# Performance work log

Measured on AMD Instinct MI355X. Metric: run time of the kernel, lower is better.

## Reference

```python
import jax, jax.numpy as jnp
import numpy as np

N = 100000   # nodes
E = 800000   # directed edges
G = 1000     # graphs
D = 128      # latent_dim
F_IN = 64    # num_node_feats
K = 3        # max_k
BLOCKS = 3   # max_block
H = 5        # multi_h_emb_weight
EPS = 1e-5


def _bn(x, g, b):
    # BatchNorm1d in training mode: biased batch variance
    m = x.mean(axis=0)
    v = x.var(axis=0)
    return (x - m) * jax.lax.rsqrt(v + EPS) * g + b


def setup_inputs() -> dict:
    key = jax.random.key(0)
    ks = jax.random.split(key, 12)
    inp = {
        'node_feat': jax.random.normal(ks[0], (N, F_IN), dtype=jnp.float32),
        'src': jax.random.randint(ks[1], (E,), 0, N),
        'dst': jax.random.randint(ks[2], (E,), 0, N),
        'seg': jnp.sort(jax.random.randint(ks[3], (N,), 0, G)),
        'node_W': jax.random.normal(ks[4], (F_IN, D), dtype=jnp.float32) * 0.05,
        'node_b': jnp.zeros((D,), jnp.float32),
        'bn1_g': jnp.ones((D,), jnp.float32),
        'bn1_b': jnp.zeros((D,), jnp.float32),
        'conv_W': jax.random.normal(ks[5], (K, D, D), dtype=jnp.float32) * 0.05,
        'conv_b': jnp.zeros((K, D), jnp.float32),
        'bn2_g': jnp.ones((K, D), jnp.float32),
        'bn2_b': jnp.zeros((K, D), jnp.float32),
        'k_weight': jax.random.normal(ks[6], (K * D, D), dtype=jnp.float32) * 0.05,
        'bn3_g': jnp.ones((D,), jnp.float32),
        'bn3_b': jnp.zeros((D,), jnp.float32),
        'attn_W1': jax.random.normal(ks[7], (D, D), dtype=jnp.float32) * 0.05,
        'attn_b1': jnp.zeros((D,), jnp.float32),
        'bna_g': jnp.ones((D,), jnp.float32),
        'bna_b': jnp.zeros((D,), jnp.float32),
        'attn_W2': jax.random.normal(ks[8], (D, H), dtype=jnp.float32) * 0.05,
        'attn_b2': jnp.zeros((H,), jnp.float32),
        'bnb_g': jnp.ones((H,), jnp.float32),
        'bnb_b': jnp.zeros((H,), jnp.float32),
    }
    return inp


def reference(node_feat, src, dst, seg,
              node_W, node_b, bn1_g, bn1_b,
              conv_W, conv_b, bn2_g, bn2_b,
              k_weight, bn3_g, bn3_b,
              attn_W1, attn_b1, bna_g, bna_b,
              attn_W2, attn_b2, bnb_g, bnb_b):
    def spmm(x):
        # torch.spmm(A, x) with unweighted n2n adjacency: out[dst] += x[src]
        return jax.ops.segment_sum(x[src], dst, num_segments=N)

    # node embedding: Linear + BN + ReLU
    inp = jax.nn.relu(_bn(node_feat @ node_W + node_b, bn1_g, bn1_b))

    cur = inp
    for block in range(BLOCKS):
        block_input = cur if block == 0 else cur + inp
        # multi_hop: K chained spmm + Linear + BN, concatenated
        input_x = block_input
        outs = []
        for k in range(K):
            pooled = spmm(input_x) + block_input
            input_x = _bn(pooled @ conv_W[k] + conv_b[k], bn2_g[k], bn2_b[k])
            outs.append(input_x)
        result = jnp.concatenate(outs, axis=-1)          # [N, K*D]
        cur = jax.nn.relu(_bn(result @ k_weight, bn3_g, bn3_b))

    node_emb = cur                                       # [N, D]

    # APooling: per-node softmax over heads, segment-wise weighted sum
    a = jnp.tanh(node_emb @ attn_W1 + attn_b1)
    a = _bn(a, bna_g, bna_b)
    a = a @ attn_W2 + attn_b2
    a = _bn(a, bnb_g, bnb_b)                             # [N, H]
    alpha = jax.nn.softmax(a, axis=-1)                   # softmax over head dim (dim=-1)
    # graph_emb[g, h, d] = sum_{n in graph g} alpha[n, h] * node_emb[n, d]
    graph_emb = jax.ops.segment_sum(alpha[:, :, None] * node_emb[:, None, :],
                                    seg, num_segments=G)  # [G, H, D]
    h_out = jax.nn.relu(graph_emb.reshape(G, H * D))

    # L1 regularizer over params with dim > 1, divided by number of graphs
    reg = (jnp.abs(node_W).sum() + jnp.abs(conv_W).sum() + jnp.abs(k_weight).sum()
           + jnp.abs(attn_W1).sum() + jnp.abs(attn_W2).sum())
    return h_out, reg / G
```

## Files before the change

kernel.cpp:

```cpp
#include <hip/hip_runtime.h>
#include <hip/hip_bf16.h>

#define D128 128
#define EPS 1e-5f

typedef unsigned short bfl;
typedef __bf16 bf16x8 __attribute__((ext_vector_type(8)));
typedef float f32x4 __attribute__((ext_vector_type(4)));

__device__ inline float bf2f(unsigned short u) { return __uint_as_float(((unsigned int)u) << 16); }
__device__ inline unsigned short f2bf(float f) {
    unsigned int x = __float_as_uint(f);
    return (unsigned short)((x + 0x7fffu + ((x >> 16) & 1u)) >> 16);
}

__global__ void dag_count_rank(const int* __restrict__ dst, int E,
                               int* __restrict__ deg, int* __restrict__ rank) {
    int i = blockIdx.x * blockDim.x + threadIdx.x;
    int stride = gridDim.x * blockDim.x;
    for (; i < E; i += stride) {
        int r = atomicAdd(&deg[dst[i]], 1);
        rank[i] = r;
    }
}

__global__ void dag_scan1(const int* __restrict__ deg, int N, int* __restrict__ out, int* __restrict__ partials) {
    __shared__ int sdata[256];
    int t = threadIdx.x;
    int base = blockIdx.x * 1024 + t * 4;
    int v[4]; int s = 0;
#pragma unroll
    for (int j = 0; j < 4; j++) { int idx = base + j; v[j] = (idx < N) ? deg[idx] : 0; s += v[j]; }
    sdata[t] = s; __syncthreads();
    for (int off = 1; off < 256; off <<= 1) {
        int x = (t >= off) ? sdata[t - off] : 0;
        __syncthreads();
        sdata[t] += x;
        __syncthreads();
    }
    int run = (t == 0) ? 0 : sdata[t - 1];
#pragma unroll
    for (int j = 0; j < 4; j++) { int idx = base + j; if (idx < N) out[idx] = run; run += v[j]; }
    if (t == 255) partials[blockIdx.x] = sdata[255];
}

__global__ void dag_scan2(int* __restrict__ partials, int P) {
    __shared__ int sdata[256];
    int t = threadIdx.x;
    int v = (t < P) ? partials[t] : 0;
    sdata[t] = v; __syncthreads();
    for (int off = 1; off < 256; off <<= 1) {
        int x = (t >= off) ? sdata[t - off] : 0;
        __syncthreads();
        sdata[t] += x;
        __syncthreads();
    }
    if (t < P) partials[t] = sdata[t] - v;
}

__global__ void dag_scan3(int* __restrict__ rowptr, const int* __restrict__ partials, int N, int E) {
    int i = blockIdx.x * blockDim.x + threadIdx.x;
    int stride = gridDim.x * blockDim.x;
    for (; i < N; i += stride) rowptr[i] += partials[i >> 10];
    if (blockIdx.x == 0 && threadIdx.x == 0) rowptr[N] = E;
}

__global__ void dag_place(const int* __restrict__ src, const int* __restrict__ dst,
                          const int* __restrict__ rank, const int* __restrict__ rowptr,
                          int E, int* __restrict__ csr_src) {
    int i = blockIdx.x * blockDim.x + threadIdx.x;
    int stride = gridDim.x * blockDim.x;
    for (; i < E; i += stride) {
        csr_src[rowptr[dst[i]] + rank[i]] = src[i];
    }
}

__global__ void dag_wconv(const float* __restrict__ node_W, const float* __restrict__ conv_W,
                          const float* __restrict__ k_weight, const float* __restrict__ attn_W1,
                          bfl* __restrict__ wt) {
    int i = blockIdx.x * blockDim.x + threadIdx.x;
    if (i >= 122880) return;
    float v;
    if (i < 8192) {
        int n = i >> 6, k = i & 63;
        v = node_W[k * 128 + n];
    } else if (i < 8192 + 49152) {
        int j = i - 8192; int k = j >> 14; int r = j & 16383;
        int n = r >> 7, kk = r & 127;
        v = conv_W[k * 16384 + kk * 128 + n];
    } else if (i < 8192 + 98304) {
        int j = i - 8192 - 49152; int k = j >> 14; int r = j & 16383;
        int n = r >> 7, kk = r & 127;
        v = k_weight[(k * 128 + kk) * 128 + n];
    } else {
        int j = i - 8192 - 98304;
        int n = j >> 7, kk = j & 127;
        v = attn_W1[kk * 128 + n];
    }
    wt[i] = f2bf(v);
}

template<bool KWPREP>
__global__ void dag_finalize(float* __restrict__ part,
                             const float* __restrict__ g, const float* __restrict__ b,
                             float invN, float* __restrict__ slot,
                             const bfl* __restrict__ WtIn, bfl* __restrict__ Wt2,
                             float* __restrict__ bias2) {
    int t = threadIdx.x;
    float acc = 0.f;
#pragma unroll
    for (int i = 0; i < 8; i++) acc += part[i * 256 + t];
#pragma unroll
    for (int i = 0; i < 8; i++) part[i * 256 + t] = 0.f;
    __shared__ float sums[256];
    __shared__ float scs[128], shs[128];
    sums[t] = acc;
    __syncthreads();
    if (t < 128) {
        float m = sums[t] * invN;
        float var = sums[128 + t] * invN - m * m;
        float scale = g[t] * rsqrtf(var + EPS);
        float shift = b[t] - m * scale;
        scs[t] = scale; shs[t] = shift;
        slot[t] = scale; slot[128 + t] = shift;
    }
    if constexpr (KWPREP) {
        __syncthreads();
        int row = t >> 1, half = t & 1;
        const bfl* wr = WtIn + row * 128 + half * 64;
        bfl* w2 = Wt2 + row * 128 + half * 64;
        float a = 0.f;
        for (int k = 0; k < 64; k += 8) {
            bf16x8 v = *(const bf16x8*)(wr + k);
            bfl o[8];
#pragma unroll
            for (int j = 0; j < 8; j++) {
                float f = (float)v[j];
                int kk = half * 64 + k + j;
                a += shs[kk] * f;
                o[j] = f2bf(scs[kk] * f);
            }
            *(bf16x8*)(w2 + k) = *(bf16x8*)o;
        }
        a += __shfl_xor(a, 1);
        if (half == 0) bias2[row] = a;
    }
}

template<int KSTEPS, int XMODE, bool BIAS, bool TANH, bool ACC, bool STATS>
__global__ __launch_bounds__(256) void gemm_rw(
        const void* __restrict__ Xv, const bfl* __restrict__ Wt,
        const float* __restrict__ bias, bfl* __restrict__ Y,
        int Nrows, float* __restrict__ partOut) {
    const int Kdim = KSTEPS * 32;
    int t = threadIdx.x;
    int lane = t & 63;
    int wave = t >> 6;
    int cg = wave & 1, rg = wave >> 1;
    int l15 = lane & 15, lg = lane >> 4;

    bf16x8 af[4][KSTEPS];
#pragma unroll
    for (int nf = 0; nf < 4; nf++)
#pragma unroll
        for (int ks = 0; ks < KSTEPS; ks++)
            af[nf][ks] = *(const bf16x8*)(Wt + (size_t)(cg * 64 + nf * 16 + l15) * Kdim + ks * 32 + lg * 8);

    float bia[4][4];
    if (BIAS) {
#pragma unroll
        for (int nf = 0; nf < 4; nf++) {
            float4 bb = *(const float4*)(bias + cg * 64 + nf * 16 + lg * 4);
            bia[nf][0] = bb.x; bia[nf][1] = bb.y; bia[nf][2] = bb.z; bia[nf][3] = bb.w;
        }
    }

    float s_c[4][4], q_c[4][4];
    if constexpr (STATS) {
#pragma unroll
        for (int nf = 0; nf < 4; nf++)
#pragma unroll
            for (int j = 0; j < 4; j++) { s_c[nf][j] = 0.f; q_c[nf][j] = 0.f; }
    }

    const int RT = (Nrows + 15) >> 4;
    const int step = gridDim.x * 2;

    auto load_bf = [&](int rt, bf16x8* bfo) {
        int r = rt * 16 + l15;
        bool valid = (rt < RT) && (r < Nrows);
#pragma unroll
        for (int ks = 0; ks < KSTEPS; ks++) {
            if (valid) {
                if (XMODE == 0) {
                    bfo[ks] = *(const bf16x8*)((const bfl*)Xv + (size_t)r * Kdim + ks * 32 + lg * 8);
                } else {
                    const float* xp = (const float*)Xv + (size_t)r * Kdim + ks * 32 + lg * 8;
                    float4 a4 = *(const float4*)xp;
                    float4 b4 = *(const float4*)(xp + 4);
                    bf16x8 bb;
                    bb[0] = (__bf16)a4.x; bb[1] = (__bf16)a4.y; bb[2] = (__bf16)a4.z; bb[3] = (__bf16)a4.w;
                    bb[4] = (__bf16)b4.x; bb[5] = (__bf16)b4.y; bb[6] = (__bf16)b4.z; bb[7] = (__bf16)b4.w;
                    bfo[ks] = bb;
                }
            } else {
                bf16x8 bb;
#pragma unroll
                for (int j = 0; j < 8; j++) bb[j] = (__bf16)0.f;
                bfo[ks] = bb;
            }
        }
    };

    auto compute_store = [&](int rt, const bf16x8* bfc) {
        int r = rt * 16 + l15;
        bool valid = (rt < RT) && (r < Nrows);
        f32x4 acc[4];
#pragma unroll
        for (int nf = 0; nf < 4; nf++) acc[nf] = (f32x4)0.f;
#pragma unroll
        for (int ks = 0; ks < KSTEPS; ks++)
#pragma unroll
            for (int nf = 0; nf < 4; nf++)
                acc[nf] = __builtin_amdgcn_mfma_f32_16x16x32_bf16(af[nf][ks], bfc[ks], acc[nf], 0, 0, 0);
#pragma unroll
        for (int nf = 0; nf < 4; nf++) {
            int c0 = cg * 64 + nf * 16 + lg * 4;
            f32x4 v = acc[nf];
            if (BIAS) {
#pragma unroll
                for (int j = 0; j < 4; j++) v[j] += bia[nf][j];
            }
            if (TANH) {
#pragma unroll
                for (int j = 0; j < 4; j++) v[j] = tanhf(v[j]);
            }
            if (valid) {
                bfl* yp = Y + (size_t)r * D128 + c0;
                if (ACC) {
                    ushort4 old = *(const ushort4*)yp;
                    v[0] += bf2f(old.x); v[1] += bf2f(old.y); v[2] += bf2f(old.z); v[3] += bf2f(old.w);
                }
                ushort4 o;
                o.x = f2bf(v[0]); o.y = f2bf(v[1]); o.z = f2bf(v[2]); o.w = f2bf(v[3]);
                *(ushort4*)yp = o;
            }
            if constexpr (STATS) {
#pragma unroll
                for (int j = 0; j < 4; j++) {
                    float f = valid ? v[j] : 0.f;
                    s_c[nf][j] += f;
                    q_c[nf][j] += f * f;
                }
            }
        }
    };

    for (int rt = blockIdx.x * 2 + rg; rt < RT; rt += 2 * step) {
        bf16x8 bfA[KSTEPS], bfB[KSTEPS];
        load_bf(rt, bfA);
        load_bf(rt + step, bfB);
        compute_store(rt, bfA);
        compute_store(rt + step, bfB);
    }

    if constexpr (STATS) {
#pragma unroll
        for (int nf = 0; nf < 4; nf++)
#pragma unroll
            for (int j = 0; j < 4; j++) {
                float s = s_c[nf][j], q = q_c[nf][j];
                s += __shfl_xor(s, 1); s += __shfl_xor(s, 2); s += __shfl_xor(s, 4); s += __shfl_xor(s, 8);
                q += __shfl_xor(q, 1); q += __shfl_xor(q, 2); q += __shfl_xor(q, 4); q += __shfl_xor(q, 8);
                s_c[nf][j] = s; q_c[nf][j] = q;
            }
        __shared__ float red[2][2][64];
        ((float*)red)[t] = 0.f;
        __syncthreads();
        if (l15 == 0) {
#pragma unroll
            for (int nf = 0; nf < 4; nf++)
#pragma unroll
                for (int j = 0; j < 4; j++) {
                    int c = nf * 16 + lg * 4 + j;
                    atomicAdd(&red[cg][0][c], s_c[nf][j]);
                    atomicAdd(&red[cg][1][c], q_c[nf][j]);
                }
        }
        __syncthreads();
        int cgi = t >> 7, stat = (t >> 6) & 1, c = t & 63;
        atomicAdd(&partOut[(size_t)(blockIdx.x & 7) * 256 + stat * 128 + cgi * 64 + c],
                  red[cgi][stat][c]);
    }
}

__global__ __launch_bounds__(256) void dag_spmm(
        const bfl* __restrict__ x, const bfl* __restrict__ bi,
        const int* __restrict__ rowptr, const int* __restrict__ csr_src,
        bfl* __restrict__ out, int N, const float* __restrict__ scsh) {
    int t = threadIdx.x;
    int lane = t & 63;
    int wave = t >> 6;
    int l16 = lane & 15;
    int sub = lane >> 4;
    int c0 = l16 * 8;
    int n = blockIdx.x * 16 + wave * 4 + sub;
    bool valid = n < N;

    float sc[8], sh[8];
    if (scsh) {
        float4 a = *(const float4*)(scsh + c0);
        float4 b = *(const float4*)(scsh + c0 + 4);
        float4 p = *(const float4*)(scsh + 128 + c0);
        float4 q = *(const float4*)(scsh + 128 + c0 + 4);
        sc[0] = a.x; sc[1] = a.y; sc[2] = a.z; sc[3] = a.w;
        sc[4] = b.x; sc[5] = b.y; sc[6] = b.z; sc[7] = b.w;
        sh[0] = p.x; sh[1] = p.y; sh[2] = p.z; sh[3] = p.w;
        sh[4] = q.x; sh[5] = q.y; sh[6] = q.z; sh[7] = q.w;
    } else {
#pragma unroll
        for (int j = 0; j < 8; j++) { sc[j] = 1.f; sh[j] = 0.f; }
    }

    int p0 = valid ? rowptr[n] : 0;
    int p1 = valid ? rowptr[n + 1] : 0;
    int deg = p1 - p0;
    int md = deg;
    md = max(md, __shfl_xor(md, 16));
    md = max(md, __shfl_xor(md, 32));

    uint4 ub = make_uint4(0, 0, 0, 0);
    if (valid) ub = *(const uint4*)(bi + (size_t)n * D128 + c0);

    const bfl* xb = x + c0;
    float acc[8];
#pragma unroll
    for (int j = 0; j < 8; j++) acc[j] = 0.f;

    for (int j = 0; j < md; j += 4) {
        uint4 u[4];
#pragma unroll
        for (int r = 0; r < 4; r++) {
            u[r] = make_uint4(0, 0, 0, 0);
            if (j + r < deg) {
                int s = csr_src[p0 + j + r];
                u[r] = *(const uint4*)(xb + (size_t)s * D128);
            }
        }
#pragma unroll
        for (int r = 0; r < 4; r++) {
            acc[0] += __uint_as_float(u[r].x << 16);
            acc[1] += __uint_as_float(u[r].x & 0xffff0000u);
            acc[2] += __uint_as_float(u[r].y << 16);
            acc[3] += __uint_as_float(u[r].y & 0xffff0000u);
            acc[4] += __uint_as_float(u[r].z << 16);
            acc[5] += __uint_as_float(u[r].z & 0xffff0000u);
            acc[6] += __uint_as_float(u[r].w << 16);
            acc[7] += __uint_as_float(u[r].w & 0xffff0000u);
        }
    }

    if (valid) {
        float cnt = (float)deg;
        float bv[8];
        bv[0] = __uint_as_float(ub.x << 16); bv[1] = __uint_as_float(ub.x & 0xffff0000u);
        bv[2] = __uint_as_float(ub.y << 16); bv[3] = __uint_as_float(ub.y & 0xffff0000u);
        bv[4] = __uint_as_float(ub.z << 16); bv[5] = __uint_as_float(ub.z & 0xffff0000u);
        bv[6] = __uint_as_float(ub.w << 16); bv[7] = __uint_as_float(ub.w & 0xffff0000u);
        float v[8];
#pragma unroll
        for (int j = 0; j < 8; j++) v[j] = sc[j] * acc[j] + cnt * sh[j] + bv[j];
        uint4 o;
        o.x = (unsigned int)f2bf(v[0]) | ((unsigned int)f2bf(v[1]) << 16);
        o.y = (unsigned int)f2bf(v[2]) | ((unsigned int)f2bf(v[3]) << 16);
        o.z = (unsigned int)f2bf(v[4]) | ((unsigned int)f2bf(v[5]) << 16);
        o.w = (unsigned int)f2bf(v[6]) | ((unsigned int)f2bf(v[7]) << 16);
        *(uint4*)(out + (size_t)n * D128 + c0) = o;
    }
}

__global__ void dag_colstat_f32(const float* __restrict__ Y, int Nrows, int C, float* __restrict__ sums) {
    __shared__ float ls[8], lss[8];
    int t = threadIdx.x;
    int nlanes = blockDim.x / C;
    int col = t % C, lane = t / C;
    float s = 0.f, ss = 0.f;
    if (lane < nlanes) {
        for (int r = blockIdx.x * nlanes + lane; r < Nrows; r += gridDim.x * nlanes) {
            float v = Y[(size_t)r * C + col];
            s += v; ss += v * v;
        }
    }
    if (t < C) { ls[t] = 0.f; lss[t] = 0.f; }
    __syncthreads();
    if (lane < nlanes) { atomicAdd(&ls[col], s); atomicAdd(&lss[col], ss); }
    __syncthreads();
    if (t < C) { atomicAdd(&sums[t], ls[t]); atomicAdd(&sums[C + t], lss[t]); }
}

template<bool RELU, bool ADDOUT, bool WRITEY>
__global__ void dag_bn_apply(bfl* __restrict__ Y, const float* __restrict__ scsh,
                             size_t n8,
                             const bfl* __restrict__ addin, bfl* __restrict__ out2) {
    __shared__ float sc[128], sh[128];
    int t = threadIdx.x;
    if (t < 128) {
        sc[t] = scsh[t];
        sh[t] = scsh[128 + t];
    }
    __syncthreads();
    for (size_t i = (size_t)blockIdx.x * blockDim.x + t; i < n8; i += (size_t)gridDim.x * blockDim.x) {
        int c0 = (int)((i * 8) & 127);
        bf16x8 v = *(bf16x8*)(Y + i * 8);
        bfl o[8], o2[8];
#pragma unroll
        for (int j = 0; j < 8; j++) {
            float f = (float)v[j] * sc[c0 + j] + sh[c0 + j];
            if (RELU) f = fmaxf(f, 0.f);
            o[j] = f2bf(f);
            if (ADDOUT) o2[j] = f2bf(f + bf2f(addin[i * 8 + j]));
        }
        if (WRITEY) *(bf16x8*)(Y + i * 8) = *(bf16x8*)o;
        if (ADDOUT) *(bf16x8*)(out2 + i * 8) = *(bf16x8*)o2;
    }
}

__global__ void dag_gemm5(const bfl* __restrict__ X, const float* __restrict__ W,
                          const float* __restrict__ bias, float* __restrict__ Y, int Nrows,
                          const float* __restrict__ scsh) {
    __shared__ float Xs[32][132];
    __shared__ float Ws[640];
    __shared__ float sc[128], sh[128];
    int t = threadIdx.x;
    if (t < 128) {
        sc[t] = scsh[t];
        sh[t] = scsh[128 + t];
    }
    for (int i = t; i < 640; i += 256) Ws[i] = W[i];
    __syncthreads();
    int row0 = blockIdx.x * 32;
#pragma unroll
    for (int i = 0; i < 2; i++) {
        int off = (i * 256 + t) * 8;
        int r = off >> 7, c = off & 127;
        int gr = row0 + r;
        if (gr < Nrows) {
            bf16x8 v = *(const bf16x8*)(X + (size_t)gr * D128 + c);
#pragma unroll
            for (int j = 0; j < 8; j++) Xs[r][c + j] = (float)v[j] * sc[c + j] + sh[c + j];
        } else {
#pragma unroll
            for (int j = 0; j < 8; j++) Xs[r][c + j] = 0.f;
        }
    }
    __syncthreads();
    if (t < 160) {
        int r = t / 5, h = t % 5;
        int gr = row0 + r;
        if (gr < Nrows) {
            float s = bias[h];
            for (int k = 0; k < 128; k++) s = fmaf(Xs[r][k], Ws[k * 5 + h], s);
            Y[(size_t)gr * 5 + h] = s;
        }
    }
}

__global__ void dag_alpha(float* __restrict__ a2, int N,
                          const float* __restrict__ sums, const float* __restrict__ g,
                          const float* __restrict__ b, float invN) {
    float scb[5], shb[5];
#pragma unroll
    for (int h = 0; h < 5; h++) {
        float s = sums[h], ss = sums[5 + h];
        float m = s * invN;
        float var = ss * invN - m * m;
        float scale = g[h] * rsqrtf(var + EPS);
        scb[h] = scale; shb[h] = b[h] - m * scale;
    }
    int n = blockIdx.x * blockDim.x + threadIdx.x;
    if (n >= N) return;
    float av[5];
    float mx = -1e30f;
#pragma unroll
    for (int h = 0; h < 5; h++) {
        av[h] = a2[(size_t)n * 5 + h] * scb[h] + shb[h];
        mx = fmaxf(mx, av[h]);
    }
    float s = 0.f;
#pragma unroll
    for (int h = 0; h < 5; h++) { av[h] = expf(av[h] - mx); s += av[h]; }
    float inv = 1.f / s;
#pragma unroll
    for (int h = 0; h < 5; h++) a2[(size_t)n * 5 + h] = av[h] * inv;
}

__global__ __launch_bounds__(256) void dag_pool(
        const float* __restrict__ alpha, const bfl* __restrict__ emb,
        const int* __restrict__ seg, int N, int G, float* __restrict__ out) {
    int gg = blockIdx.x;
    int t = threadIdx.x;
    int d = t & 127;
    int half = t >> 7;
    int lo = 0, hi = N;
    while (lo < hi) { int m = (lo + hi) >> 1; if (seg[m] < gg) lo = m + 1; else hi = m; }
    int start = lo;
    lo = start; hi = N;
    while (lo < hi) { int m = (lo + hi) >> 1; if (seg[m] < gg + 1) lo = m + 1; else hi = m; }
    int end = lo;

    float acc0[5] = {0.f, 0.f, 0.f, 0.f, 0.f};
    float acc1[5] = {0.f, 0.f, 0.f, 0.f, 0.f};
    int n = start + half;
    for (; n + 2 < end; n += 4) {
        float e0 = bf2f(emb[(size_t)n * D128 + d]);
        float e1 = bf2f(emb[(size_t)(n + 2) * D128 + d]);
#pragma unroll
        for (int h = 0; h < 5; h++) {
            acc0[h] = fmaf(alpha[(size_t)n * 5 + h], e0, acc0[h]);
            acc1[h] = fmaf(alpha[(size_t)(n + 2) * 5 + h], e1, acc1[h]);
        }
    }
    for (; n < end; n += 2) {
        float e0 = bf2f(emb[(size_t)n * D128 + d]);
#pragma unroll
        for (int h = 0; h < 5; h++)
            acc0[h] = fmaf(alpha[(size_t)n * 5 + h], e0, acc0[h]);
    }
#pragma unroll
    for (int h = 0; h < 5; h++) acc0[h] += acc1[h];

    __shared__ float red[5][128];
    if (half == 1) {
#pragma unroll
        for (int h = 0; h < 5; h++) red[h][d] = acc0[h];
    }
    __syncthreads();
    if (half == 0) {
#pragma unroll
        for (int h = 0; h < 5; h++)
            out[(size_t)gg * 640 + h * D128 + d] = fmaxf(acc0[h] + red[h][d], 0.f);
    }
}

__global__ void dag_reg(const float* w0, int n0, const float* w1, int n1, const float* w2, int n2,
                        const float* w3, int n3, const float* w4, int n4, float* out, float invG) {
    __shared__ float sd[256];
    int t = threadIdx.x;
    int gt = blockIdx.x * blockDim.x + t;
    int stride = gridDim.x * blockDim.x;
    float s = 0.f;
    const float* ws[5] = {w0, w1, w2, w3, w4};
    int ns[5] = {n0, n1, n2, n3, n4};
    for (int a = 0; a < 5; a++) {
        const float* w = ws[a]; int n = ns[a];
        for (int i = gt; i < n; i += stride) s += fabsf(w[i]);
    }
    sd[t] = s; __syncthreads();
    for (int off = 128; off > 0; off >>= 1) { if (t < off) sd[t] += sd[t + off]; __syncthreads(); }
    if (t == 0) atomicAdd(out, sd[0] * invG);
}

extern "C" void kernel_launch(void* const* d_in, const int* in_sizes, int n_in,
                              void* d_out, int out_size, void* d_ws, size_t ws_size,
                              hipStream_t stream) {
    const float* node_feat = (const float*)d_in[0];
    const int*   src       = (const int*)d_in[1];
    const int*   dst       = (const int*)d_in[2];
    const int*   seg       = (const int*)d_in[3];
    const float* node_W    = (const float*)d_in[4];
    const float* node_b    = (const float*)d_in[5];
    const float* bn1_g     = (const float*)d_in[6];
    const float* bn1_b     = (const float*)d_in[7];
    const float* conv_W    = (const float*)d_in[8];
    const float* conv_b    = (const float*)d_in[9];
    const float* bn2_g     = (const float*)d_in[10];
    const float* bn2_b     = (const float*)d_in[11];
    const float* k_weight  = (const float*)d_in[12];
    const float* bn3_g     = (const float*)d_in[13];
    const float* bn3_b     = (const float*)d_in[14];
    const float* attn_W1   = (const float*)d_in[15];
    const float* attn_b1   = (const float*)d_in[16];
    const float* bna_g     = (const float*)d_in[17];
    const float* bna_b     = (const float*)d_in[18];
    const float* attn_W2   = (const float*)d_in[19];
    const float* attn_b2   = (const float*)d_in[20];
    const float* bnb_g     = (const float*)d_in[21];
    const float* bnb_b     = (const float*)d_in[22];

    const int N = in_sizes[3];
    const int E = in_sizes[1];
    const int G = (out_size - 1) / 640;
    const int FIN = in_sizes[0] / N;
    const float invN = 1.f / (float)N;

    auto align256 = [](size_t x) { return (x + 255) & ~(size_t)255; };
    size_t NB = (size_t)N * D128 * sizeof(bfl);
    char* w = (char*)d_ws;
    bfl* P0 = (bfl*)(w + 0 * NB);
    bfl* P1 = (bfl*)(w + 1 * NB);
    bfl* P2 = (bfl*)(w + 2 * NB);
    bfl* P3 = (bfl*)(w + 3 * NB);
    bfl* P4 = (bfl*)(w + 4 * NB);
    char* tail = w + 5 * NB;
    size_t off = 0;
    int gemmGrid = (N + 127) / 128;
    float* stats = (float*)(tail + off); off = align256(off + 15 * 256 * sizeof(float));
    float* part  = (float*)(tail + off); off = align256(off + 8 * 256 * sizeof(float));
    bfl*   wt    = (bfl*)(tail + off);   off = align256(off + 122880 * sizeof(bfl));
    bfl*   wt2   = (bfl*)(tail + off);   off = align256(off + 16384 * sizeof(bfl));
    float* bias2 = (float*)(tail + off); off = align256(off + 128 * sizeof(float));
    float* a2    = (float*)(tail + off); off = align256(off + (size_t)N * 5 * sizeof(float));
    int* deg     = (int*)(tail + off);   off = align256(off + (size_t)N * 4);
    int* rowptr  = (int*)(tail + off);   off = align256(off + (size_t)(N + 1) * 4);
    int* rank    = (int*)(tail + off);   off = align256(off + (size_t)E * 4);
    int* csr_src = (int*)(tail + off);   off = align256(off + (size_t)E * 4);
    int* partials= (int*)(tail + off);   off = align256(off + 512);

    bfl* wt_node = wt;
    bfl* wt_conv = wt + 8192;
    bfl* wt_kw   = wt + 8192 + 49152;
    bfl* wt_attn = wt + 8192 + 98304;
    auto slot = [&](int s) { return stats + (size_t)s * 256; };

    int spmmGrid = (N + 15) / 16;

    hipMemsetAsync(part, 0, 8 * 256 * sizeof(float), stream);
    hipMemsetAsync(slot(14), 0, 256 * sizeof(float), stream);
    hipMemsetAsync((float*)d_out + (size_t)G * 640, 0, 4, stream);

    hipMemsetAsync(deg, 0, (size_t)N * 4, stream);
    dag_count_rank<<<1024, 256, 0, stream>>>(dst, E, deg, rank);
    int P = (N + 1023) / 1024;
    dag_scan1<<<P, 256, 0, stream>>>(deg, N, rowptr, partials);
    dag_scan2<<<1, 256, 0, stream>>>(partials, P);
    dag_scan3<<<256, 256, 0, stream>>>(rowptr, partials, N, E);
    dag_place<<<1024, 256, 0, stream>>>(src, dst, rank, rowptr, E, csr_src);

    dag_wconv<<<480, 256, 0, stream>>>(node_W, conv_W, k_weight, attn_W1, wt);

    dag_reg<<<64, 256, 0, stream>>>(node_W, FIN * D128, conv_W, 3 * D128 * D128,
                                    k_weight, 3 * D128 * D128, attn_W1, D128 * D128,
                                    attn_W2, D128 * 5, (float*)d_out + (size_t)G * 640, 1.0f / G);

    gemm_rw<2, 1, true, false, false, true><<<gemmGrid, 256, 0, stream>>>(
        node_feat, wt_node, node_b, P0, N, part);
    dag_finalize<false><<<1, 256, 0, stream>>>(part, bn1_g, bn1_b, invN,
                                               slot(0), nullptr, nullptr, nullptr);
    dag_bn_apply<true, false, true><<<2048, 256, 0, stream>>>(P0, slot(0), (size_t)N * D128 / 8,
                                                              nullptr, nullptr);

    for (int blk = 0; blk < 3; blk++) {
        const bfl* bip = (blk == 0) ? P0 : P1;
        for (int k = 0; k < 3; k++) {
            int s2i = 1 + blk * 3 + k;
            const bfl* in_x = (k == 0) ? bip : P4;
            const float* s2 = (k == 0) ? nullptr : slot(s2i - 1);
            dag_spmm<<<spmmGrid, 256, 0, stream>>>(in_x, bip, rowptr, csr_src, P3, N, s2);
            gemm_rw<4, 0, true, false, false, true><<<gemmGrid, 256, 0, stream>>>(
                P3, wt_conv + (size_t)k * 16384, conv_b + k * D128, P4, N, part);
            dag_finalize<true><<<1, 256, 0, stream>>>(part,
                                                      bn2_g + k * D128, bn2_b + k * D128, invN,
                                                      slot(s2i), wt_kw + (size_t)k * 16384, wt2, bias2);
            if (k == 0)
                gemm_rw<4, 0, true, false, false, false><<<gemmGrid, 256, 0, stream>>>(
                    P4, wt2, bias2, P2, N, nullptr);
            else if (k == 1)
                gemm_rw<4, 0, true, false, true, false><<<gemmGrid, 256, 0, stream>>>(
                    P4, wt2, bias2, P2, N, nullptr);
            else
                gemm_rw<4, 0, true, false, true, true><<<gemmGrid, 256, 0, stream>>>(
                    P4, wt2, bias2, P2, N, part);
        }
        dag_finalize<false><<<1, 256, 0, stream>>>(part, bn3_g, bn3_b, invN,
                                                   slot(10 + blk), nullptr, nullptr, nullptr);
        if (blk < 2)
            dag_bn_apply<true, true, false><<<2048, 256, 0, stream>>>(P2, slot(10 + blk),
                                                                      (size_t)N * D128 / 8, P0, P1);
        else
            dag_bn_apply<true, false, true><<<2048, 256, 0, stream>>>(P2, slot(10 + blk),
                                                                      (size_t)N * D128 / 8, nullptr, nullptr);
    }

    gemm_rw<4, 0, true, true, false, true><<<gemmGrid, 256, 0, stream>>>(
        P2, wt_attn, attn_b1, P3, N, part);
    dag_finalize<false><<<1, 256, 0, stream>>>(part, bna_g, bna_b, invN,
                                               slot(13), nullptr, nullptr, nullptr);
    dag_gemm5<<<(N + 31) / 32, 256, 0, stream>>>(P3, attn_W2, attn_b2, a2, N, slot(13));
    dag_colstat_f32<<<256, 255, 0, stream>>>(a2, N, 5, slot(14));
    dag_alpha<<<(N + 255) / 256, 256, 0, stream>>>(a2, N, slot(14), bnb_g, bnb_b, invN);
    dag_pool<<<G, 256, 0, stream>>>(a2, P2, seg, N, G, (float*)d_out);
}
```

Baseline: 1.132 ms.

## Defer k_weight projection into single fused three-input GEMM per block

When workspace allows a sixth activation buffer, each conv output k is stored separately and its BN-folded k_weight slice saved. A new kernel then computes the whole concatenated projection in one pass and accumulates BN statistics. This removes two launches per block and the repeated read-modify-write of the accumulation buffer. It costs one extra N×D buffer and uses a fallback path when the workspace is too small.

Measured after the change: 1.202 ms. +6.2%, slower.

```diff
diff --git a/kernel.cpp b/kernel.cpp
--- a/kernel.cpp
+++ b/kernel.cpp
@@ -292,6 +292,121 @@
         atomicAdd(&partOut[(size_t)(blockIdx.x & 7) * 256 + stat * 128 + cgi * 64 + c],
                   red[cgi][stat][c]);
     }
+}
+
+__global__ __launch_bounds__(256) void gemm_kw3(
+        const bfl* __restrict__ O0, const bfl* __restrict__ O1, const bfl* __restrict__ O2,
+        const bfl* __restrict__ wt3, const float* __restrict__ b3,
+        bfl* __restrict__ Y, int Nrows, float* __restrict__ partOut) {
+    int t = threadIdx.x;
+    int lane = t & 63;
+    int wave = t >> 6;
+    int cg = wave & 1, rg = wave >> 1;
+    int l15 = lane & 15, lg = lane >> 4;
+
+    float bia[4][4];
+#pragma unroll
+    for (int nf = 0; nf < 4; nf++) {
+        int c0 = cg * 64 + nf * 16 + lg * 4;
+        float4 b0 = *(const float4*)(b3 + c0);
+        float4 b1 = *(const float4*)(b3 + 128 + c0);
+        float4 b2 = *(const float4*)(b3 + 256 + c0);
+        bia[nf][0] = b0.x + b1.x + b2.x;
+        bia[nf][1] = b0.y + b1.y + b2.y;
+        bia[nf][2] = b0.z + b1.z + b2.z;
+        bia[nf][3] = b0.w + b1.w + b2.w;
+    }
+
+    float s_c[4][4], q_c[4][4];
+#pragma unroll
+    for (int nf = 0; nf < 4; nf++)
+#pragma unroll
+        for (int j = 0; j < 4; j++) { s_c[nf][j] = 0.f; q_c[nf][j] = 0.f; }
+
+    const bfl* Xs[3] = {O0, O1, O2};
+    const int RT = (Nrows + 15) >> 4;
+    const int step = gridDim.x * 2;
+
+    for (int rt = blockIdx.x * 2 + rg; rt < RT; rt += step) {
+        int r = rt * 16 + l15;
+        bool valid = r < Nrows;
+        f32x4 acc[4];
+#pragma unroll
+        for (int nf = 0; nf < 4; nf++) acc[nf] = (f32x4)0.f;
+#pragma unroll 1
+        for (int c = 0; c < 3; c++) {
+            const bfl* Wt = wt3 + (size_t)c * 16384;
+            const bfl* X = Xs[c];
+            bf16x8 af[4][4];
+#pragma unroll
+            for (int nf = 0; nf < 4; nf++)
+#pragma unroll
+                for (int ks = 0; ks < 4; ks++)
+                    af[nf][ks] = *(const bf16x8*)(Wt + (size_t)(cg * 64 + nf * 16 + l15) * D128 + ks * 32 + lg * 8);
+            bf16x8 bf[4];
+#pragma unroll
+            for (int ks = 0; ks < 4; ks++) {
+                if (valid) bf[ks] = *(const bf16x8*)(X + (size_t)r * D128 + ks * 32 + lg * 8);
+                else {
+                    bf16x8 bb;
+#pragma unroll
+                    for (int j = 0; j < 8; j++) bb[j] = (__bf16)0.f;
+                    bf[ks] = bb;
+                }
+            }
+#pragma unroll
+            for (int ks = 0; ks < 4; ks++)
+#pragma unroll
+                for (int nf = 0; nf < 4; nf++)
+                    acc[nf] = __builtin_amdgcn_mfma_f32_16x16x32_bf16(af[nf][ks], bf[ks], acc[nf], 0, 0, 0);
+        }
+#pragma unroll
+        for (int nf = 0; nf < 4; nf++) {
+            int c0 = cg * 64 + nf * 16 + lg * 4;
+            f32x4 v = acc[nf];
+#pragma unroll
+            for (int j = 0; j < 4; j++) v[j] += bia[nf][j];
+            if (valid) {
+                bfl* yp = Y + (size_t)r * D128 + c0;
+                ushort4 o;
+                o.x = f2bf(v[0]); o.y = f2bf(v[1]); o.z = f2bf(v[2]); o.w = f2bf(v[3]);
+                *(ushort4*)yp = o;
+            }
+#pragma unroll
+            for (int j = 0; j < 4; j++) {
+                float f = valid ? v[j] : 0.f;
+                s_c[nf][j] += f;
+                q_c[nf][j] += f * f;
+            }
+        }
+    }
+
+#pragma unroll
+    for (int nf = 0; nf < 4; nf++)
+#pragma unroll
+        for (int j = 0; j < 4; j++) {
+            float s = s_c[nf][j], q = q_c[nf][j];
+            s += __shfl_xor(s, 1); s += __shfl_xor(s, 2); s += __shfl_xor(s, 4); s += __shfl_xor(s, 8);
+            q += __shfl_xor(q, 1); q += __shfl_xor(q, 2); q += __shfl_xor(q, 4); q += __shfl_xor(q, 8);
+            s_c[nf][j] = s; q_c[nf][j] = q;
+        }
+    __shared__ float red[2][2][64];
+    ((float*)red)[t] = 0.f;
+    __syncthreads();
+    if (l15 == 0) {
+#pragma unroll
+        for (int nf = 0; nf < 4; nf++)
+#pragma unroll
+            for (int j = 0; j < 4; j++) {
+                int c = nf * 16 + lg * 4 + j;
+                atomicAdd(&red[cg][0][c], s_c[nf][j]);
+                atomicAdd(&red[cg][1][c], q_c[nf][j]);
+            }
+    }
+    __syncthreads();
+    int cgi = t >> 7, stat = (t >> 6) & 1, c = t & 63;
+    atomicAdd(&partOut[(size_t)(blockIdx.x & 7) * 256 + stat * 128 + cgi * 64 + c],
+              red[cgi][stat][c]);
 }
 
 __global__ __launch_bounds__(256) void dag_spmm(
@@ -595,26 +710,43 @@
 
     auto align256 = [](size_t x) { return (x + 255) & ~(size_t)255; };
     size_t NB = (size_t)N * D128 * sizeof(bfl);
+
+    size_t toff = 0;
+    size_t o_stats = toff; toff = align256(toff + 15 * 256 * sizeof(float));
+    size_t o_part  = toff; toff = align256(toff + 8 * 256 * sizeof(float));
+    size_t o_wt    = toff; toff = align256(toff + 122880 * sizeof(bfl));
+    size_t o_wt3   = toff; toff = align256(toff + 3 * 16384 * sizeof(bfl));
+    size_t o_b3    = toff; toff = align256(toff + 3 * 128 * sizeof(float));
+    size_t o_a2    = toff; toff = align256(toff + (size_t)N * 5 * sizeof(float));
+    size_t o_deg   = toff; toff = align256(toff + (size_t)N * 4);
+    size_t o_rp    = toff; toff = align256(toff + (size_t)(N + 1) * 4);
+    size_t o_rank  = toff; toff = align256(toff + (size_t)E * 4);
+    size_t o_csr   = toff; toff = align256(toff + (size_t)E * 4);
+    size_t o_prt   = toff; toff = align256(toff + 512);
+
+    size_t need6 = 6 * NB + toff;
+    bool deferred = (ws_size >= need6);
+    int nbuf = deferred ? 6 : 5;
+
     char* w = (char*)d_ws;
     bfl* P0 = (bfl*)(w + 0 * NB);
     bfl* P1 = (bfl*)(w + 1 * NB);
     bfl* P2 = (bfl*)(w + 2 * NB);
     bfl* P3 = (bfl*)(w + 3 * NB);
     bfl* P4 = (bfl*)(w + 4 * NB);
-    char* tail = w + 5 * NB;
-    size_t off = 0;
-    int gemmGrid = (N + 127) / 128;
-    float* stats = (float*)(tail + off); off = align256(off + 15 * 256 * sizeof(float));
-    float* part  = (float*)(tail + off); off = align256(off + 8 * 256 * sizeof(float));
-    bfl*   wt    = (bfl*)(tail + off);   off = align256(off + 122880 * sizeof(bfl));
-    bfl*   wt2   = (bfl*)(tail + off);   off = align256(off + 16384 * sizeof(bfl));
-    float* bias2 = (float*)(tail + off); off = align256(off + 128 * sizeof(float));
-    float* a2    = (float*)(tail + off); off = align256(off + (size_t)N * 5 * sizeof(float));
-    int* deg     = (int*)(tail + off);   off = align256(off + (size_t)N * 4);
-    int* rowptr  = (int*)(tail + off);   off = align256(off + (size_t)(N + 1) * 4);
-    int* rank    = (int*)(tail + off);   off = align256(off + (size_t)E * 4);
-    int* csr_src = (int*)(tail + off);   off = align256(off + (size_t)E * 4);
-    int* partials= (int*)(tail + off);   off = align256(off + 512);
+    bfl* P5 = deferred ? (bfl*)(w + 5 * NB) : nullptr;
+    char* tail = w + nbuf * NB;
+    float* stats = (float*)(tail + o_stats);
+    float* part  = (float*)(tail + o_part);
+    bfl*   wt    = (bfl*)(tail + o_wt);
+    bfl*   wt3   = (bfl*)(tail + o_wt3);
+    float* b3    = (float*)(tail + o_b3);
+    float* a2    = (float*)(tail + o_a2);
+    int* deg     = (int*)(tail + o_deg);
+    int* rowptr  = (int*)(tail + o_rp);
+    int* rank    = (int*)(tail + o_rank);
+    int* csr_src = (int*)(tail + o_csr);
+    int* partials= (int*)(tail + o_prt);
 
     bfl* wt_node = wt;
     bfl* wt_conv = wt + 8192;
@@ -622,6 +754,7 @@
     bfl* wt_attn = wt + 8192 + 98304;
     auto slot = [&](int s) { return stats + (size_t)s * 256; };
 
+    int gemmGrid = (N + 127) / 128;
     int spmmGrid = (N + 15) / 16;
 
     hipMemsetAsync(part, 0, 8 * 256 * sizeof(float), stream);
@@ -651,25 +784,43 @@
 
     for (int blk = 0; blk < 3; blk++) {
         const bfl* bip = (blk == 0) ? P0 : P1;
-        for (int k = 0; k < 3; k++) {
-            int s2i = 1 + blk * 3 + k;
-            const bfl* in_x = (k == 0) ? bip : P4;
-            const float* s2 = (k == 0) ? nullptr : slot(s2i - 1);
-            dag_spmm<<<spmmGrid, 256, 0, stream>>>(in_x, bip, rowptr, csr_src, P3, N, s2);
-            gemm_rw<4, 0, true, false, false, true><<<gemmGrid, 256, 0, stream>>>(
-                P3, wt_conv + (size_t)k * 16384, conv_b + k * D128, P4, N, part);
-            dag_finalize<true><<<1, 256, 0, stream>>>(part,
-                                                      bn2_g + k * D128, bn2_b + k * D128, invN,
-                                                      slot(s2i), wt_kw + (size_t)k * 16384, wt2, bias2);
-            if (k == 0)
-                gemm_rw<4, 0, true, false, false, false><<<gemmGrid, 256, 0, stream>>>(
-                    P4, wt2, bias2, P2, N, nullptr);
-            else if (k == 1)
-                gemm_rw<4, 0, true, false, true, false><<<gemmGrid, 256, 0, stream>>>(
-                    P4, wt2, bias2, P2, N, nullptr);
-            else
-                gemm_rw<4, 0, true, false, true, true><<<gemmGrid, 256, 0, stream>>>(
-                    P4, wt2, bias2, P2, N, part);
+        if (deferred) {
+            bfl* Obuf[3] = {P3, P4, P5};
+            for (int k = 0; k < 3; k++) {
+                int s2i = 1 + blk * 3 + k;
+                const bfl* in_x = (k == 0) ? bip : Obuf[k - 1];
+                const float* s2 = (k == 0) ? nullptr : slot(s2i - 1);
+                dag_spmm<<<spmmGrid, 256, 0, stream>>>(in_x, bip, rowptr, csr_src, P2, N, s2);
+                gemm_rw<4, 0, true, false, false, true><<<gemmGrid, 256, 0, stream>>>(
+                    P2, wt_conv + (size_t)k * 16384, conv_b + k * D128, Obuf[k], N, part);
+                dag_finalize<true><<<1, 256, 0, stream>>>(part,
+                                                          bn2_g + k * D128, bn2_b + k * D128, invN,
+                                                          slot(s2i), wt_kw + (size_t)k * 16384,
+                                                          wt3 + (size_t)k * 16384, b3 + k * 128);
+            }
+            gemm_kw3<<<gemmGrid, 256, 0, stream>>>(P3, P4, P5, wt3, b3, P2, N, part);
+        } else {
+            for (int k = 0; k < 3; k++) {
+                int s2i = 1 + blk * 3 + k;
+                const bfl* in_x = (k == 0) ? bip : P4;
+                const float* s2 = (k == 0) ? nullptr : slot(s2i - 1);
+                dag_spmm<<<spmmGrid, 256, 0, stream>>>(in_x, bip, rowptr, csr_src, P3, N, s2);
+                gemm_rw<4, 0, true, false, false, true><<<gemmGrid, 256, 0, stream>>>(
+                    P3, wt_conv + (size_t)k * 16384, conv_b + k * D128, P4, N, part);
+                dag_finalize<true><<<1, 256, 0, stream>>>(part,
+                                                          bn2_g + k * D128, bn2_b + k * D128, invN,
+                                                          slot(s2i), wt_kw + (size_t)k * 16384,
+                                                          wt3, b3);
+                if (k == 0)
+                    gemm_rw<4, 0, true, false, false, false><<<gemmGrid, 256, 0, stream>>>(
+                        P4, wt3, b3, P2, N, nullptr);
+                else if (k == 1)
+                    gemm_rw<4, 0, true, false, true, false><<<gemmGrid, 256, 0, stream>>>(
+                        P4, wt3, b3, P2, N, nullptr);
+                else
+                    gemm_rw<4, 0, true, false, true, true><<<gemmGrid, 256, 0, stream>>>(
+                        P4, wt3, b3, P2, N, part);
+            }
         }
         dag_finalize<false><<<1, 256, 0, stream>>>(part, bn3_g, bn3_b, invN,
                                                    slot(10 + blk), nullptr, nullptr, nullptr);
```
